# Performance work log

Measured on AMD Instinct MI355X. Metric: run time of the kernel, lower is better.

The kernel has to match this reference:

```python
import jax, jax.numpy as jnp
import numpy as np

D = 256      # cfg.d_model
H = 8        # num heads
HID = D // H # head_outdim for hidden layers (32)
N = 16000    # nodes
E = 64000    # edges
NUM_GNN = 3  # cfg.num_gnn -> 2 hidden EGATConv layers + 1 final
SLOPE = 0.01 # F.leaky_relu default in DGL EGATConv


def setup_inputs() -> dict:
    key = jax.random.key(0)
    ks = jax.random.split(key, 8)
    inp = {
        "nfeat": jax.random.normal(ks[0], (N, D), jnp.float32),
        "efeat": jax.random.normal(ks[1], (E, D), jnp.float32),
        "src": jax.random.randint(ks[2], (E,), 0, N),
        "dst": jax.random.randint(ks[3], (E,), 0, N),
    }
    L = NUM_GNN - 1  # hidden layers, out_node = out_edge = HID per head
    kh = jax.random.split(ks[4], 5)
    s = 0.02
    inp["Wnode_h"] = jax.random.normal(kh[0], (L, D, H * HID), jnp.float32) * s
    inp["Wni_h"]   = jax.random.normal(kh[1], (L, D, H * HID), jnp.float32) * s
    inp["Wnj_h"]   = jax.random.normal(kh[2], (L, D, H * HID), jnp.float32) * s
    inp["Wfij_h"]  = jax.random.normal(kh[3], (L, D, H * HID), jnp.float32) * s
    inp["attn_h"]  = jax.random.normal(kh[4], (L, H, HID), jnp.float32) * s
    inp["bias_h"]  = jnp.zeros((L, H * HID), jnp.float32)
    kl = jax.random.split(ks[5], 5)
    inp["Wnode_l"] = jax.random.normal(kl[0], (D, H * D), jnp.float32) * s
    inp["Wni_l"]   = jax.random.normal(kl[1], (D, H * D), jnp.float32) * s
    inp["Wnj_l"]   = jax.random.normal(kl[2], (D, H * D), jnp.float32) * s
    inp["Wfij_l"]  = jax.random.normal(kl[3], (D, H * D), jnp.float32) * s
    inp["attn_l"]  = jax.random.normal(kl[4], (H, D), jnp.float32) * s
    inp["bias_l"]  = jnp.zeros((H * D,), jnp.float32)
    return inp


def _egat(n, f, src, dst, Wnode, Wni, Wnj, Wfij, attn, bias):
    """DGL EGATConv: edge-gated multi-head graph attention.
    n:[N,D] f:[E,D] attn:[H,od] -> (h_out:[N,H,od], f_out:[E,H,od])."""
    Hh, od = attn.shape
    # edge feature update: f_ni(u) + f_nj(v) + f_fij(e) + bias, leaky_relu
    f_out = (n @ Wni)[src] + (n @ Wnj)[dst] + f @ Wfij + bias  # [E, H*od]
    f_out = jax.nn.leaky_relu(f_out, SLOPE).reshape(-1, Hh, od)
    # attention logits + edge softmax grouped by destination node
    e = jnp.einsum('ehd,hd->eh', f_out, attn)                   # [E, H]
    m = jax.lax.stop_gradient(jax.ops.segment_max(e, dst, num_segments=N))
    ex = jnp.exp(e - m[dst])
    s = jax.ops.segment_sum(ex, dst, num_segments=N)
    a = ex / s[dst]                                             # [E, H]
    # message passing: u_mul_e + sum at dst
    h = (n @ Wnode).reshape(N, Hh, od)
    h_out = jax.ops.segment_sum(h[src] * a[..., None], dst, num_segments=N)
    return h_out, f_out


def reference(nfeat, efeat, src, dst,
              Wnode_h, Wni_h, Wnj_h, Wfij_h, attn_h, bias_h,
              Wnode_l, Wni_l, Wnj_l, Wfij_l, attn_l, bias_l):
    n, f = nfeat, efeat
    for l in range(Wnode_h.shape[0]):  # hidden layers: concat heads + ELU + residual
        tn, tf = _egat(n, f, src, dst, Wnode_h[l], Wni_h[l], Wnj_h[l],
                       Wfij_h[l], attn_h[l], bias_h[l])
        n = n + jax.nn.elu(tn.reshape(N, -1))  # reshape == concat over heads
        f = f + jax.nn.elu(tf.reshape(E, -1))
    # last layer: mean over heads + residual
    tn, tf = _egat(n, f, src, dst, Wnode_l, Wni_l, Wnj_l, Wfij_l, attn_l, bias_l)
    n = n + tn.mean(axis=1)
    f = f + tf.mean(axis=1)
    return n, f
```

## Files before the change

### kernel.cpp

```cpp
#include <hip/hip_runtime.h>

typedef unsigned short u16;
typedef __attribute__((ext_vector_type(4))) unsigned short u16x4;
typedef __attribute__((ext_vector_type(8))) unsigned short u16x8;
typedef __attribute__((ext_vector_type(4))) float f32x4;
typedef __attribute__((ext_vector_type(8))) __bf16 bf16x8;

#define NN 16000
#define NE 64000

__device__ __forceinline__ float bf2f(u16 b) {
  union { unsigned int u; float f; } v; v.u = ((unsigned int)b) << 16; return v.f;
}
__device__ __forceinline__ u16 f2bf(float x) {
  union { float f; unsigned int u; } v; v.f = x;
  unsigned int r = v.u + 0x7FFFu + ((v.u >> 16) & 1u);
  return (u16)(r >> 16);
}

__global__ void cast_init(const float* __restrict__ in, float* __restrict__ outf,
                          u16* __restrict__ outb, int n4) {
  for (int i = blockIdx.x * blockDim.x + threadIdx.x; i < n4; i += gridDim.x * blockDim.x) {
    f32x4 v = ((const f32x4*)in)[i];
    u16x4 b;
#pragma unroll
    for (int j = 0; j < 4; ++j) b[j] = f2bf(v[j]);
    ((f32x4*)outf)[i] = v;
    ((u16x4*)outb)[i] = b;
  }
}

__global__ void cast_bf(const float* __restrict__ in, u16* __restrict__ outb, int n4) {
  for (int i = blockIdx.x * blockDim.x + threadIdx.x; i < n4; i += gridDim.x * blockDim.x) {
    f32x4 v = ((const f32x4*)in)[i];
    u16x4 b;
#pragma unroll
    for (int j = 0; j < 4; ++j) b[j] = f2bf(v[j]);
    ((u16x4*)outb)[i] = b;
  }
}

__global__ void deg_hist(const int* __restrict__ dst, int* __restrict__ deg) {
  int e = blockIdx.x * 256 + threadIdx.x;
  if (e < NE) atomicAdd(&deg[dst[e]], 1);
}

__global__ __launch_bounds__(1024) void scan_deg(const int* __restrict__ deg,
                                                 int* __restrict__ row_ptr,
                                                 int* __restrict__ cursor) {
  __shared__ int lds[1024];
  int t = threadIdx.x;
  int base = t * 16;
  int v[16];
  int s = 0;
#pragma unroll
  for (int j = 0; j < 16; ++j) {
    int idx = base + j;
    v[j] = idx < NN ? deg[idx] : 0;
    s += v[j];
  }
  lds[t] = s;
  __syncthreads();
  for (int d = 1; d < 1024; d <<= 1) {
    int x = t >= d ? lds[t - d] : 0;
    __syncthreads();
    lds[t] += x;
    __syncthreads();
  }
  int run = lds[t] - s;
  for (int j = 0; j < 16; ++j) {
    int idx = base + j;
    if (idx < NN) { row_ptr[idx] = run; cursor[idx] = run; run += v[j]; }
  }
  if (t == 1023) row_ptr[NN] = run;
}

__global__ void csr_fill(const int* __restrict__ src, const int* __restrict__ dst,
                         int* __restrict__ cursor, int* __restrict__ cs_e,
                         int* __restrict__ cs_src) {
  int e = blockIdx.x * 256 + threadIdx.x;
  if (e >= NE) return;
  int pos = atomicAdd(&cursor[dst[e]], 1);
  cs_e[pos] = e;
  cs_src[pos] = src[e];
}

__global__ void transpose4(const float* __restrict__ W0, const float* __restrict__ W1,
                           const float* __restrict__ W2, const float* __restrict__ W3,
                           int ld, int osz, u16* __restrict__ WT) {
  __shared__ float t[16][17];
  int z = blockIdx.z;
  const float* W = z == 0 ? W0 : (z == 1 ? W1 : (z == 2 ? W2 : W3));
  u16* O = WT + (size_t)z * osz;
  int n0 = blockIdx.x * 16, k0 = blockIdx.y * 16;
  int tx = threadIdx.x, ty = threadIdx.y;
  t[ty][tx] = W[(size_t)(k0 + ty) * ld + n0 + tx];
  __syncthreads();
  O[(size_t)(n0 + ty) * 256 + k0 + tx] = f2bf(t[tx][ty]);
}

__global__ __launch_bounds__(256) void gemm_abt(
    const u16* __restrict__ A,
    const u16* __restrict__ BT0, const u16* __restrict__ BT1, const u16* __restrict__ BT2,
    u16* __restrict__ C0, u16* __restrict__ C1, u16* __restrict__ C2, int ldc) {
  const int bz = blockIdx.z;
  const u16* BT = bz == 0 ? BT0 : (bz == 1 ? BT1 : BT2);
  u16* C = bz == 0 ? C0 : (bz == 1 ? C1 : C2);
  const int nx = gridDim.x;
  const int nwg = nx * gridDim.y;
  int bid = blockIdx.y * nx + blockIdx.x;
  int q = nwg >> 3, r = nwg & 7;
  int xcd = bid & 7, idx = bid >> 3;
  int wg = (xcd < r) ? (xcd * (q + 1) + idx) : (r * (q + 1) + (xcd - r) * q + idx);
  const int m0 = (wg / nx) * 128;
  const int n0 = (wg % nx) * 128;
  __shared__ __attribute__((aligned(16))) char smem[69632];
  u16* lA = (u16*)smem;
  u16* lB = (u16*)(smem + 32768);
  const int tid = threadIdx.x;
  const int lane = tid & 63;
  const int wid = tid >> 6;
  const int wr = (wid >> 1) * 64;
  const int wc = (wid & 1) * 64;
  const int srow = tid >> 3;
  const int sdst = (tid & 7) * 8;
  const int ssrc = (((tid & 7) ^ (srow & 7))) * 8;
  const int sx = (lane >> 4) ^ (lane & 7);
  f32x4 acc[4][4] = {};
#define STAGE(buf, kb)                                                                         \
  {                                                                                            \
    _Pragma("unroll") for (int i = 0; i < 4; ++i) {                                            \
      const int row = srow + i * 32;                                                           \
      __builtin_amdgcn_global_load_lds(                                                        \
          (const __attribute__((address_space(1))) void*)(A + (size_t)(m0 + row) * 256 + (kb) + ssrc), \
          (__attribute__((address_space(3))) void*)(lA + (buf) * 8192 + row * 64 + sdst), 16, 0, 0); \
      __builtin_amdgcn_global_load_lds(                                                        \
          (const __attribute__((address_space(1))) void*)(BT + (size_t)(n0 + row) * 256 + (kb) + ssrc), \
          (__attribute__((address_space(3))) void*)(lB + (buf) * 8192 + row * 64 + sdst), 16, 0, 0); \
    }                                                                                          \
  }
  STAGE(0, 0)
  __syncthreads();
#pragma unroll
  for (int t = 0; t < 4; ++t) {
    if (t < 3) STAGE((t + 1) & 1, (t + 1) * 64)
    const u16* pA = lA + (t & 1) * 8192;
    const u16* pB = lB + (t & 1) * 8192;
#pragma unroll
    for (int kk = 0; kk < 2; ++kk) {
      const int sw = ((kk << 2) ^ sx) * 8;
      bf16x8 af[4], bfr[4];
#pragma unroll
      for (int m = 0; m < 4; ++m)
        af[m] = *(const bf16x8*)(pA + (wr + m * 16 + (lane & 15)) * 64 + sw);
#pragma unroll
      for (int n = 0; n < 4; ++n)
        bfr[n] = *(const bf16x8*)(pB + (wc + n * 16 + (lane & 15)) * 64 + sw);
#pragma unroll
      for (int m = 0; m < 4; ++m)
#pragma unroll
        for (int n = 0; n < 4; ++n)
          acc[m][n] = __builtin_amdgcn_mfma_f32_16x16x32_bf16(af[m], bfr[n], acc[m][n], 0, 0, 0);
    }
    __syncthreads();
  }
#undef STAGE
  const int cr = (lane >> 4) * 4;
  const int cc = lane & 15;
  float* stg = (float*)smem + wid * (64 * 68);
#pragma unroll
  for (int m = 0; m < 4; ++m)
#pragma unroll
    for (int n = 0; n < 4; ++n)
#pragma unroll
      for (int j = 0; j < 4; ++j)
        stg[(m * 16 + cr + j) * 68 + n * 16 + cc] = acc[m][n][j];
  const int rr = lane >> 3;
  const int c0 = (lane & 7) * 8;
#pragma unroll
  for (int p = 0; p < 8; ++p) {
    int row = p * 8 + rr;
    f32x4 v0 = *(const f32x4*)(stg + row * 68 + c0);
    f32x4 v1 = *(const f32x4*)(stg + row * 68 + c0 + 4);
    u16x8 o;
#pragma unroll
    for (int i = 0; i < 4; ++i) { o[i] = f2bf(v0[i]); o[4 + i] = f2bf(v1[i]); }
    *(u16x8*)(&C[(size_t)(m0 + wr + row) * ldc + (n0 + wc + c0)]) = o;
  }
}

__global__ __launch_bounds__(256) void edge_hidden(
    const u16* __restrict__ t3, const u16* __restrict__ fW,
    const int* __restrict__ src, const int* __restrict__ dst,
    const float* __restrict__ bias, const float* __restrict__ attn,
    u16* __restrict__ f_bf, float* __restrict__ exb) {
  int e = blockIdx.x * 4 + (threadIdx.x >> 6);
  if (e >= NE) return;
  int lane = threadIdx.x & 63;
  int is = src[e], id = dst[e];
  int c = lane * 4;
  u16x4 va = *(const u16x4*)(t3 + (size_t)is * 768 + c);
  u16x4 vb = *(const u16x4*)(t3 + (size_t)id * 768 + 256 + c);
  u16x4 vc = *(const u16x4*)(fW + (size_t)e * 256 + c);
  f32x4 vbi = *(const f32x4*)(bias + c);
  int h = lane >> 3;
  f32x4 vat = *(const f32x4*)(attn + h * 32 + (lane & 7) * 4);
  size_t idx0 = (size_t)e * 256 + c;
  u16x4 fo = *(u16x4*)(f_bf + idx0);
  float part = 0.f;
#pragma unroll
  for (int j = 0; j < 4; ++j) {
    float y = bf2f(va[j]) + bf2f(vb[j]) + bf2f(vc[j]) + vbi[j];
    y = y > 0.f ? y : 0.01f * y;
    part += y * vat[j];
    float el = y > 0.f ? y : expm1f(y);
    fo[j] = f2bf(bf2f(fo[j]) + el);
  }
  *(u16x4*)(f_bf + idx0) = fo;
  part += __shfl_xor(part, 1);
  part += __shfl_xor(part, 2);
  part += __shfl_xor(part, 4);
  part = fminf(fmaxf(part, -30.f), 30.f);
  if ((lane & 7) == 0) exb[(size_t)e * 8 + h] = expf(part);
}

__global__ __launch_bounds__(256) void node_gather_hidden(
    const u16* __restrict__ t3, const int* __restrict__ row_ptr,
    const int* __restrict__ cs_e, const int* __restrict__ cs_src,
    const float* __restrict__ exb, float* __restrict__ n_cur, u16* __restrict__ n_bf) {
  int node = blockIdx.x * 4 + (threadIdx.x >> 6);
  if (node >= NN) return;
  int lane = threadIdx.x & 63;
  int c = lane * 4, h = lane >> 3;
  int beg = row_ptr[node], end = row_ptr[node + 1];
  float denom = 0.f;
  float acc[4] = {0.f, 0.f, 0.f, 0.f};
  for (int p = beg; p < end; ++p) {
    float a = exb[(size_t)cs_e[p] * 8 + h];
    denom += a;
    u16x4 hv = *(const u16x4*)(t3 + (size_t)cs_src[p] * 768 + 512 + c);
#pragma unroll
    for (int j = 0; j < 4; ++j) acc[j] += a * bf2f(hv[j]);
  }
  float inv = denom > 0.f ? 1.f / denom : 0.f;
  size_t i0 = (size_t)node * 256 + c;
  f32x4 nv = *(f32x4*)(n_cur + i0);
  u16x4 bv;
#pragma unroll
  for (int j = 0; j < 4; ++j) {
    float t = acc[j] * inv;
    t = t > 0.f ? t : expm1f(t);
    nv[j] += t;
    bv[j] = f2bf(nv[j]);
  }
  *(f32x4*)(n_cur + i0) = nv;
  *(u16x4*)(n_bf + i0) = bv;
}

__global__ __launch_bounds__(256) void edge_final_all(
    int e0, int nech, const u16* __restrict__ t_ni, const u16* __restrict__ t_nj,
    const u16* __restrict__ fWc, const int* __restrict__ src, const int* __restrict__ dst,
    const float* __restrict__ bias, const float* __restrict__ attn,
    const u16* __restrict__ f_bf, float* __restrict__ out_f, float* __restrict__ exb) {
  int ec = blockIdx.x * 4 + (threadIdx.x >> 6);
  if (ec >= nech) return;
  int e = e0 + ec;
  int lane = threadIdx.x & 63;
  int is = src[e], id = dst[e];
  int c = lane * 4;
  float total[4] = {0.f, 0.f, 0.f, 0.f};
#pragma unroll
  for (int h = 0; h < 8; ++h) {
    u16x4 va = *(const u16x4*)(t_ni + (size_t)is * 2048 + h * 256 + c);
    u16x4 vb = *(const u16x4*)(t_nj + (size_t)id * 2048 + h * 256 + c);
    u16x4 vc = *(const u16x4*)(fWc + (size_t)ec * 2048 + h * 256 + c);
    f32x4 vbi = *(const f32x4*)(bias + h * 256 + c);
    f32x4 vat = *(const f32x4*)(attn + h * 256 + c);
    float part = 0.f;
#pragma unroll
    for (int j = 0; j < 4; ++j) {
      float y = bf2f(va[j]) + bf2f(vb[j]) + bf2f(vc[j]) + vbi[j];
      y = y > 0.f ? y : 0.01f * y;
      part += y * vat[j];
      total[j] += 0.125f * y;
    }
#pragma unroll
    for (int m = 1; m < 64; m <<= 1) part += __shfl_xor(part, m);
    part = fminf(fmaxf(part, -30.f), 30.f);
    if (lane == 0) exb[(size_t)e * 8 + h] = expf(part);
  }
  size_t i0 = (size_t)e * 256 + c;
  u16x4 fs = *(const u16x4*)(f_bf + i0);
  f32x4 o;
#pragma unroll
  for (int j = 0; j < 4; ++j) o[j] = bf2f(fs[j]) + total[j];
  *(f32x4*)(out_f + i0) = o;
}

__global__ __launch_bounds__(256) void node_gather_final_all(
    const u16* __restrict__ t_node, const int* __restrict__ row_ptr,
    const int* __restrict__ cs_e, const int* __restrict__ cs_src,
    const float* __restrict__ exb, const float* __restrict__ n_cur,
    float* __restrict__ out_n) {
  int node = blockIdx.x * 4 + (threadIdx.x >> 6);
  if (node >= NN) return;
  int lane = threadIdx.x & 63;
  int c = lane * 4;
  int beg = row_ptr[node], end = row_ptr[node + 1];
  float dh[8] = {};
  float acc[8][4] = {};
  for (int p = beg; p < end; ++p) {
    int e = cs_e[p];
    int s = cs_src[p];
    const u16* rowb = t_node + (size_t)s * 2048;
    const float* eb = exb + (size_t)e * 8;
    float a[8];
    u16x4 rv[8];
#pragma unroll
    for (int h = 0; h < 8; ++h) {
      a[h] = eb[h];
      rv[h] = *(const u16x4*)(rowb + h * 256 + c);
    }
#pragma unroll
    for (int h = 0; h < 8; ++h) {
      dh[h] += a[h];
#pragma unroll
      for (int j = 0; j < 4; ++j) acc[h][j] += a[h] * bf2f(rv[h][j]);
    }
  }
  float total[4] = {0.f, 0.f, 0.f, 0.f};
#pragma unroll
  for (int h = 0; h < 8; ++h) {
    float inv = dh[h] > 0.f ? 0.125f / dh[h] : 0.f;
#pragma unroll
    for (int j = 0; j < 4; ++j) total[j] += acc[h][j] * inv;
  }
  size_t i0 = (size_t)node * 256 + c;
  f32x4 nv = *(const f32x4*)(n_cur + i0);
#pragma unroll
  for (int j = 0; j < 4; ++j) nv[j] += total[j];
  *(f32x4*)(out_n + i0) = nv;
}

extern "C" void kernel_launch(void* const* d_in, const int* in_sizes, int n_in,
                              void* d_out, int out_size, void* d_ws, size_t ws_size,
                              hipStream_t stream) {
  const float* nfeat   = (const float*)d_in[0];
  const float* efeat   = (const float*)d_in[1];
  const int*   src     = (const int*)d_in[2];
  const int*   dst     = (const int*)d_in[3];
  const float* Wnode_h = (const float*)d_in[4];
  const float* Wni_h   = (const float*)d_in[5];
  const float* Wnj_h   = (const float*)d_in[6];
  const float* Wfij_h  = (const float*)d_in[7];
  const float* attn_h  = (const float*)d_in[8];
  const float* bias_h  = (const float*)d_in[9];
  const float* Wnode_l = (const float*)d_in[10];
  const float* Wni_l   = (const float*)d_in[11];
  const float* Wnj_l   = (const float*)d_in[12];
  const float* Wfij_l  = (const float*)d_in[13];
  const float* attn_l  = (const float*)d_in[14];
  const float* bias_l  = (const float*)d_in[15];

  char* ws = (char*)d_ws;
  size_t off = 0;
  auto alloc = [&](size_t b) { char* p = ws + off; off += (b + 255) & ~(size_t)255; return p; };
  float* n_cur = (float*)alloc((size_t)NN * 256 * 4);
  u16* n_bf    = (u16*)alloc((size_t)NN * 256 * 2);
  u16* f_bf    = (u16*)alloc((size_t)NE * 256 * 2);
  u16* t_ni    = (u16*)alloc((size_t)NN * 2048 * 2);
  u16* t_nj    = (u16*)alloc((size_t)NN * 2048 * 2);
  u16* t_node  = (u16*)alloc((size_t)NN * 2048 * 2);
  float* exb   = (float*)alloc((size_t)NE * 8 * 4);
  u16* WT      = (u16*)alloc((size_t)4 * 65536 * 2);
  u16* WTF     = (u16*)alloc((size_t)4 * 524288 * 2);
  int* deg     = (int*)alloc((size_t)NN * 4);
  int* cursor  = (int*)alloc((size_t)NN * 4);
  int* row_ptr = (int*)alloc((size_t)(NN + 1) * 4);
  int* cs_e    = (int*)alloc((size_t)NE * 4);
  int* cs_src  = (int*)alloc((size_t)NE * 4);
  int ech;
  u16* fW;
  size_t fw_big = (size_t)16000 * 2048 * 2;
  size_t fw_small = (size_t)NE * 256 * 2;
  if (off + fw_big <= ws_size) { ech = 16000; fW = (u16*)alloc(fw_big); }
  else                         { ech = 6400;  fW = (u16*)alloc(fw_small); }

  u16* WT_fij  = WT + 3 * 65536;
  u16* WTF_node = WTF;
  u16* WTF_ni   = WTF + (size_t)1 * 524288;
  u16* WTF_nj   = WTF + (size_t)2 * 524288;
  u16* WTF_fij  = WTF + (size_t)3 * 524288;

  float* out_n = (float*)d_out;
  float* out_f = out_n + (size_t)NN * 256;

  hipMemsetAsync(deg, 0, (size_t)NN * 4, stream);
  deg_hist<<<(NE + 255) / 256, 256, 0, stream>>>(dst, deg);
  scan_deg<<<1, 1024, 0, stream>>>(deg, row_ptr, cursor);
  csr_fill<<<(NE + 255) / 256, 256, 0, stream>>>(src, dst, cursor, cs_e, cs_src);

  cast_init<<<1024, 256, 0, stream>>>(nfeat, n_cur, n_bf, NN * 256 / 4);
  cast_bf<<<2048, 256, 0, stream>>>(efeat, f_bf, NE * 256 / 4);

  for (int l = 0; l < 2; ++l) {
    transpose4<<<dim3(16, 16, 4), dim3(16, 16), 0, stream>>>(
        Wni_h + (size_t)l * 65536, Wnj_h + (size_t)l * 65536,
        Wnode_h + (size_t)l * 65536, Wfij_h + (size_t)l * 65536, 256, 65536, WT);
    gemm_abt<<<dim3(6, 125, 1), 256, 0, stream>>>(n_bf, WT, WT, WT,
                                                  t_ni, t_ni, t_ni, 768);
    gemm_abt<<<dim3(2, 500, 1), 256, 0, stream>>>(f_bf, WT_fij, WT_fij, WT_fij,
                                                  fW, fW, fW, 256);
    edge_hidden<<<16000, 256, 0, stream>>>(t_ni, fW, src, dst,
        bias_h + (size_t)l * 256, attn_h + (size_t)l * 256, f_bf, exb);
    node_gather_hidden<<<4000, 256, 0, stream>>>(t_ni, row_ptr, cs_e, cs_src, exb, n_cur, n_bf);
  }

  transpose4<<<dim3(128, 16, 4), dim3(16, 16), 0, stream>>>(
      Wnode_l, Wni_l, Wnj_l, Wfij_l, 2048, 524288, WTF);
  gemm_abt<<<dim3(16, 125, 3), 256, 0, stream>>>(n_bf, WTF_ni, WTF_nj, WTF_node,
                                                 t_ni, t_nj, t_node, 2048);
  for (int e0 = 0; e0 < NE; e0 += ech) {
    const u16* Ac = f_bf + (size_t)e0 * 256;
    gemm_abt<<<dim3(16, ech / 128, 1), 256, 0, stream>>>(Ac, WTF_fij, WTF_fij, WTF_fij,
                                                         fW, fW, fW, 2048);
    edge_final_all<<<ech / 4, 256, 0, stream>>>(e0, ech, t_ni, t_nj, fW, src, dst,
                                                bias_l, attn_l, f_bf, out_f, exb);
  }
  node_gather_final_all<<<4000, 256, 0, stream>>>(t_node, row_ptr, cs_e, cs_src,
                                                  exb, n_cur, out_n);
}
```

Measured before the change: 662.5 us.

## Fuse final-layer edge GEMM with edge epilogue using head-interleaved weight layout

The final layer's weight columns are permuted so that the 8 heads of each output channel sit next to each other. This lets the edge GEMM epilogue add the gathered ni/nj rows, bias and leaky-relu, then take the head mean in registers and write out_f directly. The goal is to avoid the round trip of the 64000x2048 bf16 fW intermediate through memory and the separate edge_final_all pass. Attention logits are now written as per-tile partial sums and combined in a small logit_reduce kernel, and the node gather reads the interleaved t_node rows with wider loads. The cost is an extra partial-sum buffer and kernel, plus more complex epilogue gathers with scattered scalar stores to out_f.

After: 660.3 us. No clear change (-0.3%).

```diff
diff --git a/kernel.cpp b/kernel.cpp
--- a/kernel.cpp
+++ b/kernel.cpp
@@ -8,6 +8,7 @@
 
 #define NN 16000
 #define NE 64000
+#define ECH 16000
 
 __device__ __forceinline__ float bf2f(u16 b) {
   union { unsigned int u; float f; } v; v.u = ((unsigned int)b) << 16; return v.f;
@@ -97,6 +98,30 @@
   t[ty][tx] = W[(size_t)(k0 + ty) * ld + n0 + tx];
   __syncthreads();
   O[(size_t)(n0 + ty) * 256 + k0 + tx] = f2bf(t[tx][ty]);
+}
+
+__global__ void transpose4p(const float* __restrict__ W0, const float* __restrict__ W1,
+                            const float* __restrict__ W2, const float* __restrict__ W3,
+                            u16* __restrict__ WT) {
+  __shared__ float t[16][17];
+  int z = blockIdx.z;
+  const float* W = z == 0 ? W0 : (z == 1 ? W1 : (z == 2 ? W2 : W3));
+  u16* O = WT + (size_t)z * 524288;
+  int n0 = blockIdx.x * 16, k0 = blockIdx.y * 16;
+  int tx = threadIdx.x, ty = threadIdx.y;
+  t[ty][tx] = W[(size_t)(k0 + ty) * 2048 + n0 + tx];
+  __syncthreads();
+  int n = n0 + ty;
+  int j = (n & 255) * 8 + (n >> 8);
+  O[(size_t)j * 256 + k0 + tx] = f2bf(t[tx][ty]);
+}
+
+__global__ void permute_ba(const float* __restrict__ bias, const float* __restrict__ attn,
+                           float* __restrict__ bias_p, float* __restrict__ attn_p) {
+  int n = blockIdx.x * 256 + threadIdx.x;
+  int j = (n & 255) * 8 + (n >> 8);
+  bias_p[j] = bias[n];
+  attn_p[j] = attn[n];
 }
 
 __global__ __launch_bounds__(256) void gemm_abt(
@@ -189,6 +214,139 @@
   }
 }
 
+__global__ __launch_bounds__(256) void gemm_fused_final(
+    int e0, const u16* __restrict__ A, const u16* __restrict__ BT,
+    const u16* __restrict__ t_ni, const u16* __restrict__ t_nj,
+    const int* __restrict__ src, const int* __restrict__ dst,
+    const float* __restrict__ bias_p, const float* __restrict__ attn_p,
+    const u16* __restrict__ f_bf, float* __restrict__ out_f, float* __restrict__ part) {
+  const int nx = gridDim.x;
+  const int nwg = nx * gridDim.y;
+  int bid = blockIdx.y * nx + blockIdx.x;
+  int q = nwg >> 3, r = nwg & 7;
+  int xcd = bid & 7, idx = bid >> 3;
+  int wg = (xcd < r) ? (xcd * (q + 1) + idx) : (r * (q + 1) + (xcd - r) * q + idx);
+  const int m0 = (wg / nx) * 128;
+  const int n0 = (wg % nx) * 128;
+  __shared__ __attribute__((aligned(16))) char smem[69632];
+  u16* lA = (u16*)smem;
+  u16* lB = (u16*)(smem + 32768);
+  const int tid = threadIdx.x;
+  const int lane = tid & 63;
+  const int wid = tid >> 6;
+  const int wr = (wid >> 1) * 64;
+  const int wc = (wid & 1) * 64;
+  const int srow = tid >> 3;
+  const int sdst = (tid & 7) * 8;
+  const int ssrc = (((tid & 7) ^ (srow & 7))) * 8;
+  const int sx = (lane >> 4) ^ (lane & 7);
+  f32x4 acc[4][4] = {};
+#define STAGE(buf, kb)                                                                         \
+  {                                                                                            \
+    _Pragma("unroll") for (int i = 0; i < 4; ++i) {                                            \
+      const int row = srow + i * 32;                                                           \
+      __builtin_amdgcn_global_load_lds(                                                        \
+          (const __attribute__((address_space(1))) void*)(A + (size_t)(m0 + row) * 256 + (kb) + ssrc), \
+          (__attribute__((address_space(3))) void*)(lA + (buf) * 8192 + row * 64 + sdst), 16, 0, 0); \
+      __builtin_amdgcn_global_load_lds(                                                        \
+          (const __attribute__((address_space(1))) void*)(BT + (size_t)(n0 + row) * 256 + (kb) + ssrc), \
+          (__attribute__((address_space(3))) void*)(lB + (buf) * 8192 + row * 64 + sdst), 16, 0, 0); \
+    }                                                                                          \
+  }
+  STAGE(0, 0)
+  __syncthreads();
+#pragma unroll
+  for (int t = 0; t < 4; ++t) {
+    if (t < 3) STAGE((t + 1) & 1, (t + 1) * 64)
+    const u16* pA = lA + (t & 1) * 8192;
+    const u16* pB = lB + (t & 1) * 8192;
+#pragma unroll
+    for (int kk = 0; kk < 2; ++kk) {
+      const int sw = ((kk << 2) ^ sx) * 8;
+      bf16x8 af[4], bfr[4];
+#pragma unroll
+      for (int m = 0; m < 4; ++m)
+        af[m] = *(const bf16x8*)(pA + (wr + m * 16 + (lane & 15)) * 64 + sw);
+#pragma unroll
+      for (int n = 0; n < 4; ++n)
+        bfr[n] = *(const bf16x8*)(pB + (wc + n * 16 + (lane & 15)) * 64 + sw);
+#pragma unroll
+      for (int m = 0; m < 4; ++m)
+#pragma unroll
+        for (int n = 0; n < 4; ++n)
+          acc[m][n] = __builtin_amdgcn_mfma_f32_16x16x32_bf16(af[m], bfr[n], acc[m][n], 0, 0, 0);
+    }
+    __syncthreads();
+  }
+#undef STAGE
+  const int cr = (lane >> 4) * 4;
+  const int cc = lane & 15;
+  float* stg = (float*)smem + wid * (64 * 68);
+#pragma unroll
+  for (int m = 0; m < 4; ++m)
+#pragma unroll
+    for (int n = 0; n < 4; ++n)
+#pragma unroll
+      for (int j = 0; j < 4; ++j)
+        stg[(m * 16 + cr + j) * 68 + n * 16 + cc] = acc[m][n][j];
+  const int rr = lane >> 3;
+  const int c0 = (lane & 7) * 8;
+  const int j0 = n0 + wc + c0;
+  const int cmod = j0 >> 3;
+  const int wgrp = (n0 + wc) >> 6;
+  f32x4 bias0 = *(const f32x4*)(bias_p + j0);
+  f32x4 bias1 = *(const f32x4*)(bias_p + j0 + 4);
+  f32x4 attn0 = *(const f32x4*)(attn_p + j0);
+  f32x4 attn1 = *(const f32x4*)(attn_p + j0 + 4);
+#pragma unroll 4
+  for (int p = 0; p < 8; ++p) {
+    int row = p * 8 + rr;
+    int er = m0 + wr + row;
+    int e = e0 + er;
+    int is = src[e], id = dst[e];
+    f32x4 v0 = *(const f32x4*)(stg + row * 68 + c0);
+    f32x4 v1 = *(const f32x4*)(stg + row * 68 + c0 + 4);
+    u16x8 ni8 = *(const u16x8*)(t_ni + (size_t)is * 2048 + j0);
+    u16x8 nj8 = *(const u16x8*)(t_nj + (size_t)id * 2048 + j0);
+    float y[8];
+#pragma unroll
+    for (int h = 0; h < 4; ++h) {
+      float t0 = v0[h] + bf2f(ni8[h]) + bf2f(nj8[h]) + bias0[h];
+      y[h] = t0 > 0.f ? t0 : 0.01f * t0;
+      float t1 = v1[h] + bf2f(ni8[4 + h]) + bf2f(nj8[4 + h]) + bias1[h];
+      y[4 + h] = t1 > 0.f ? t1 : 0.01f * t1;
+    }
+    float outv = 0.125f * (((y[0] + y[1]) + (y[2] + y[3])) + ((y[4] + y[5]) + (y[6] + y[7])));
+    out_f[(size_t)e * 256 + cmod] = outv + bf2f(f_bf[(size_t)e * 256 + cmod]);
+    float lp[8];
+#pragma unroll
+    for (int h = 0; h < 4; ++h) { lp[h] = y[h] * attn0[h]; lp[4 + h] = y[4 + h] * attn1[h]; }
+#pragma unroll
+    for (int mask = 1; mask < 8; mask <<= 1)
+#pragma unroll
+      for (int h = 0; h < 8; ++h) lp[h] += __shfl_xor(lp[h], mask);
+    if ((lane & 7) == 0)
+#pragma unroll
+      for (int h = 0; h < 8; ++h) part[(size_t)er * 256 + h * 32 + wgrp] = lp[h];
+  }
+}
+
+__global__ __launch_bounds__(256) void logit_reduce(
+    int e0, const float* __restrict__ part, float* __restrict__ exb) {
+  int er = blockIdx.x * 4 + (threadIdx.x >> 6);
+  if (er >= ECH) return;
+  int lane = threadIdx.x & 63;
+  int h = lane >> 3;
+  int w4 = (lane & 7) * 4;
+  f32x4 v = *(const f32x4*)(part + (size_t)er * 256 + h * 32 + w4);
+  float s = (v[0] + v[1]) + (v[2] + v[3]);
+  s += __shfl_xor(s, 1);
+  s += __shfl_xor(s, 2);
+  s += __shfl_xor(s, 4);
+  s = fminf(fmaxf(s, -30.f), 30.f);
+  if ((lane & 7) == 0) exb[(size_t)(e0 + er) * 8 + h] = expf(s);
+}
+
 __global__ __launch_bounds__(256) void edge_hidden(
     const u16* __restrict__ t3, const u16* __restrict__ fW,
     const int* __restrict__ src, const int* __restrict__ dst,
@@ -257,46 +415,6 @@
   *(u16x4*)(n_bf + i0) = bv;
 }
 
-__global__ __launch_bounds__(256) void edge_final_all(
-    int e0, int nech, const u16* __restrict__ t_ni, const u16* __restrict__ t_nj,
-    const u16* __restrict__ fWc, const int* __restrict__ src, const int* __restrict__ dst,
-    const float* __restrict__ bias, const float* __restrict__ attn,
-    const u16* __restrict__ f_bf, float* __restrict__ out_f, float* __restrict__ exb) {
-  int ec = blockIdx.x * 4 + (threadIdx.x >> 6);
-  if (ec >= nech) return;
-  int e = e0 + ec;
-  int lane = threadIdx.x & 63;
-  int is = src[e], id = dst[e];
-  int c = lane * 4;
-  float total[4] = {0.f, 0.f, 0.f, 0.f};
-#pragma unroll
-  for (int h = 0; h < 8; ++h) {
-    u16x4 va = *(const u16x4*)(t_ni + (size_t)is * 2048 + h * 256 + c);
-    u16x4 vb = *(const u16x4*)(t_nj + (size_t)id * 2048 + h * 256 + c);
-    u16x4 vc = *(const u16x4*)(fWc + (size_t)ec * 2048 + h * 256 + c);
-    f32x4 vbi = *(const f32x4*)(bias + h * 256 + c);
-    f32x4 vat = *(const f32x4*)(attn + h * 256 + c);
-    float part = 0.f;
-#pragma unroll
-    for (int j = 0; j < 4; ++j) {
-      float y = bf2f(va[j]) + bf2f(vb[j]) + bf2f(vc[j]) + vbi[j];
-      y = y > 0.f ? y : 0.01f * y;
-      part += y * vat[j];
-      total[j] += 0.125f * y;
-    }
-#pragma unroll
-    for (int m = 1; m < 64; m <<= 1) part += __shfl_xor(part, m);
-    part = fminf(fmaxf(part, -30.f), 30.f);
-    if (lane == 0) exb[(size_t)e * 8 + h] = expf(part);
-  }
-  size_t i0 = (size_t)e * 256 + c;
-  u16x4 fs = *(const u16x4*)(f_bf + i0);
-  f32x4 o;
-#pragma unroll
-  for (int j = 0; j < 4; ++j) o[j] = bf2f(fs[j]) + total[j];
-  *(f32x4*)(out_f + i0) = o;
-}
-
 __global__ __launch_bounds__(256) void node_gather_final_all(
     const u16* __restrict__ t_node, const int* __restrict__ row_ptr,
     const int* __restrict__ cs_e, const int* __restrict__ cs_src,
@@ -312,20 +430,19 @@
   for (int p = beg; p < end; ++p) {
     int e = cs_e[p];
     int s = cs_src[p];
-    const u16* rowb = t_node + (size_t)s * 2048;
+    const u16* rowb = t_node + (size_t)s * 2048 + (size_t)c * 8;
     const float* eb = exb + (size_t)e * 8;
     float a[8];
-    u16x4 rv[8];
-#pragma unroll
-    for (int h = 0; h < 8; ++h) {
-      a[h] = eb[h];
-      rv[h] = *(const u16x4*)(rowb + h * 256 + c);
-    }
+    u16x8 rv[4];
+#pragma unroll
+    for (int h = 0; h < 8; ++h) a[h] = eb[h];
+#pragma unroll
+    for (int jj = 0; jj < 4; ++jj) rv[jj] = *(const u16x8*)(rowb + jj * 8);
 #pragma unroll
     for (int h = 0; h < 8; ++h) {
       dh[h] += a[h];
 #pragma unroll
-      for (int j = 0; j < 4; ++j) acc[h][j] += a[h] * bf2f(rv[h][j]);
+      for (int jj = 0; jj < 4; ++jj) acc[h][jj] += a[h] * bf2f(rv[jj][h]);
     }
   }
   float total[4] = {0.f, 0.f, 0.f, 0.f};
@@ -333,12 +450,12 @@
   for (int h = 0; h < 8; ++h) {
     float inv = dh[h] > 0.f ? 0.125f / dh[h] : 0.f;
 #pragma unroll
-    for (int j = 0; j < 4; ++j) total[j] += acc[h][j] * inv;
+    for (int jj = 0; jj < 4; ++jj) total[jj] += acc[h][jj] * inv;
   }
   size_t i0 = (size_t)node * 256 + c;
   f32x4 nv = *(const f32x4*)(n_cur + i0);
 #pragma unroll
-  for (int j = 0; j < 4; ++j) nv[j] += total[j];
+  for (int jj = 0; jj < 4; ++jj) nv[jj] += total[jj];
   *(f32x4*)(out_n + i0) = nv;
 }
 
@@ -374,17 +491,15 @@
   float* exb   = (float*)alloc((size_t)NE * 8 * 4);
   u16* WT      = (u16*)alloc((size_t)4 * 65536 * 2);
   u16* WTF     = (u16*)alloc((size_t)4 * 524288 * 2);
+  u16* fW      = (u16*)alloc((size_t)NE * 256 * 2);
+  float* part  = (float*)alloc((size_t)ECH * 256 * 4);
+  float* biasp = (float*)alloc(2048 * 4);
+  float* attnp = (float*)alloc(2048 * 4);
   int* deg     = (int*)alloc((size_t)NN * 4);
   int* cursor  = (int*)alloc((size_t)NN * 4);
   int* row_ptr = (int*)alloc((size_t)(NN + 1) * 4);
   int* cs_e    = (int*)alloc((size_t)NE * 4);
   int* cs_src  = (int*)alloc((size_t)NE * 4);
-  int ech;
-  u16* fW;
-  size_t fw_big = (size_t)16000 * 2048 * 2;
-  size_t fw_small = (size_t)NE * 256 * 2;
-  if (off + fw_big <= ws_size) { ech = 16000; fW = (u16*)alloc(fw_big); }
-  else                         { ech = 6400;  fW = (u16*)alloc(fw_small); }
 
   u16* WT_fij  = WT + 3 * 65536;
   u16* WTF_node = WTF;
@@ -416,16 +531,16 @@
     node_gather_hidden<<<4000, 256, 0, stream>>>(t_ni, row_ptr, cs_e, cs_src, exb, n_cur, n_bf);
   }
 
-  transpose4<<<dim3(128, 16, 4), dim3(16, 16), 0, stream>>>(
-      Wnode_l, Wni_l, Wnj_l, Wfij_l, 2048, 524288, WTF);
+  transpose4p<<<dim3(128, 16, 4), dim3(16, 16), 0, stream>>>(
+      Wnode_l, Wni_l, Wnj_l, Wfij_l, WTF);
+  permute_ba<<<8, 256, 0, stream>>>(bias_l, attn_l, biasp, attnp);
   gemm_abt<<<dim3(16, 125, 3), 256, 0, stream>>>(n_bf, WTF_ni, WTF_nj, WTF_node,
                                                  t_ni, t_nj, t_node, 2048);
-  for (int e0 = 0; e0 < NE; e0 += ech) {
-    const u16* Ac = f_bf + (size_t)e0 * 256;
-    gemm_abt<<<dim3(16, ech / 128, 1), 256, 0, stream>>>(Ac, WTF_fij, WTF_fij, WTF_fij,
-                                                         fW, fW, fW, 2048);
-    edge_final_all<<<ech / 4, 256, 0, stream>>>(e0, ech, t_ni, t_nj, fW, src, dst,
-                                                bias_l, attn_l, f_bf, out_f, exb);
+  for (int e0 = 0; e0 < NE; e0 += ECH) {
+    gemm_fused_final<<<dim3(16, ECH / 128), 256, 0, stream>>>(
+        e0, f_bf + (size_t)e0 * 256, WTF_fij, t_ni, t_nj, src, dst,
+        biasp, attnp, f_bf, out_f, part);
+    logit_reduce<<<ECH / 4, 256, 0, stream>>>(e0, part, exb);
   }
   node_gather_final_all<<<4000, 256, 0, stream>>>(t_node, row_ptr, cs_e, cs_src,
                                                   exb, n_cur, out_n);
```
